# Performance work log

Hardware: AMD Instinct MI355X
Metric: run time of the kernel (lower is better)

The kernel has to match this reference:

```python
import jax, jax.numpy as jnp
import numpy as np

B, T, I, H, C = 8192, 28, 28, 128, 10


def setup_inputs() -> dict:
    key = jax.random.key(0)
    ks = jax.random.split(key, 7)
    s_ih = 1.0 / np.sqrt(H)
    return {
        "x": jax.random.normal(ks[0], (B, T, I), dtype=jnp.float32),
        "W_ih": jax.random.normal(ks[1], (4 * H, I), dtype=jnp.float32) * s_ih,
        "W_hh": jax.random.normal(ks[2], (4 * H, H), dtype=jnp.float32) * s_ih,
        "b_ih": jax.random.normal(ks[3], (4 * H,), dtype=jnp.float32) * s_ih,
        "b_hh": jax.random.normal(ks[4], (4 * H,), dtype=jnp.float32) * s_ih,
        "W_fc": jax.random.normal(ks[5], (C, H), dtype=jnp.float32) * s_ih,
        "b_fc": jnp.zeros((C,), dtype=jnp.float32),
    }


def reference(x, W_ih, W_hh, b_ih, b_hh, W_fc, b_fc):
    # x: [B, T, I]. PyTorch LSTM gate order: i, f, g, o.
    b = b_ih + b_hh  # [4H]
    # Precompute input projections for all timesteps: [T, B, 4H]
    x_proj = jnp.einsum("bti,gi->tbg", x, W_ih) + b
    h0 = jnp.zeros((x.shape[0], H), dtype=x.dtype)
    c0 = jnp.zeros_like(h0)

    def step(carry, xp_t):
        h, c = carry
        gates = xp_t + h @ W_hh.T  # [B, 4H]
        i_g, f_g, g_g, o_g = jnp.split(gates, 4, axis=-1)
        i_g = jax.nn.sigmoid(i_g)
        f_g = jax.nn.sigmoid(f_g)
        g_g = jnp.tanh(g_g)
        o_g = jax.nn.sigmoid(o_g)
        c = f_g * c + i_g * g_g
        h = o_g * jnp.tanh(c)
        return (h, c), None

    (h_last, _), _ = jax.lax.scan(step, (h0, c0), x_proj)
    # outputs[:, -1, :] == final hidden state; fc + relu
    return jax.nn.relu(h_last @ W_fc.T + b_fc)
```

## Files before the change

kernel.cpp:

```cpp
#include <hip/hip_runtime.h>
#include <math.h>

typedef __attribute__((ext_vector_type(8))) _Float16 half8;
typedef __attribute__((ext_vector_type(4))) _Float16 half4;
typedef __attribute__((ext_vector_type(4))) float    f32x4;
typedef __attribute__((ext_vector_type(2))) float    f32x2;

#define TSTEPS 28
#define IDIM   28
#define HDIM   128
#define NKC    5
#define TILE_B 32
#define CDIM   10

#if __has_builtin(__builtin_amdgcn_exp2f)
#define EXP2F(x) __builtin_amdgcn_exp2f(x)
#else
#define EXP2F(x) exp2f(x)
#endif
#if __has_builtin(__builtin_amdgcn_rcpf)
#define RCPF(x) __builtin_amdgcn_rcpf(x)
#else
#define RCPF(x) (1.0f / (x))
#endif

#define NLOG2E (-1.44269504f)
#define P2LOG2E (2.88539008f)

__global__ __launch_bounds__(256) void pack_w(const float* __restrict__ Wih,
                                              const float* __restrict__ Whh,
                                              const float* __restrict__ bih,
                                              const float* __restrict__ bhh,
                                              _Float16* __restrict__ P) {
    int e = blockIdx.x * 256 + threadIdx.x;
    if (e >= NKC * 4 * 8 * 64 * 8) return;
    int j  = e & 7;
    int ln = (e >> 3) & 63;
    int w  = (e >> 9) & 7;
    int t  = (e >> 12) & 3;
    int kc = e >> 14;
    int k  = kc * 32 + ((ln >> 4) << 3) + j;
    int u  = w * 16 + (ln & 15);
    int g  = t * HDIM + u;
    float v = 0.f;
    if (k < HDIM)                   v = Whh[g * HDIM + k];
    else if (k < HDIM + IDIM)       v = Wih[g * IDIM + (k - HDIM)];
    else if (k == HDIM + IDIM)      v = bih[g] + bhh[g];
    float sc = (t == 2) ? P2LOG2E : NLOG2E;
    P[e] = (_Float16)(v * sc);
}

__global__ __launch_bounds__(512, 2) void lstm_kernel(
    const float* __restrict__ x,
    const _Float16* __restrict__ P,
    const float* __restrict__ Wfc,
    const float* __restrict__ b_fc,
    float* __restrict__ out)
{
    __shared__ __align__(16) _Float16 frag[2][NKC][64][8];
    __shared__ __align__(16) float hplain[TILE_B][HDIM + 4];

    const int tid = threadIdx.x;
    const int l   = tid & 63;
    const int w   = tid >> 6;
    const int b0  = blockIdx.x * TILE_B;

    half8 breg[4][4];
    half8 breg4[4];
    {
        const half8* Pp = (const half8*)P;
        #pragma unroll
        for (int kc = 0; kc < 4; ++kc)
            #pragma unroll
            for (int t4 = 0; t4 < 4; ++t4)
                breg[t4][kc] = Pp[((kc * 4 + t4) * 8 + w) * 64 + l];
        #pragma unroll
        for (int t4 = 0; t4 < 4; ++t4)
            breg4[t4] = Pp[((4 * 4 + t4) * 8 + w) * 64 + l];
    }

    {
        float4 z = {0.f, 0.f, 0.f, 0.f};
        if (tid < 256) {
            ((float4*)frag)[tid] = z;
            ((float4*)frag)[320 + tid] = z;
        }
    }
    if (tid < 32) {
        int g = tid >> 4, i = tid & 15;
        half4 onev = {(_Float16)1.f, (_Float16)0.f, (_Float16)0.f, (_Float16)0.f};
        *(half4*)&frag[g][4][48 + i][4] = onev;
    }

    const bool xact = (l < 14);
    const int xid   = w * 14 + l;
    const int xrow  = xid / 7, xg = xid % 7;
    const int xslot = xrow + 16 * (xg >> 1);
    const int xoff  = (xg & 1) * 4;
    const float4* xsA = (const float4*)(x + (size_t)(b0 + xrow) * (TSTEPS * IDIM));
    const float4* xsB = (const float4*)(x + (size_t)(b0 + 16 + xrow) * (TSTEPS * IDIM));
    float4 xh;
    if (xact) {
        float4 xa0 = xsA[xg];
        float4 xb0 = xsB[xg];
        half4 ha = {(_Float16)xa0.x, (_Float16)xa0.y, (_Float16)xa0.z, (_Float16)xa0.w};
        half4 hb = {(_Float16)xb0.x, (_Float16)xb0.y, (_Float16)xb0.z, (_Float16)xb0.w};
        *(half4*)&frag[0][4][xslot][xoff] = ha;
        *(half4*)&frag[1][4][xslot][xoff] = hb;
        xh = xsA[7 + xg];
    }

    f32x2 cA01 = {0.f, 0.f}, cA23 = {0.f, 0.f};
    f32x2 cB01 = {0.f, 0.f}, cB23 = {0.f, 0.f};
    const int u    = w * 16 + (l & 15);
    const int kc_h = w >> 1;
    const int quad = (2 * w + ((l >> 3) & 1)) & 3;
    const int jh   = l & 7;
    const int mb   = (l >> 4) << 2;

    f32x4 acc_A[4], acc_B[4];

    auto activation = [&](f32x4 (&g4)[4], f32x2 &c01, f32x2 &c23,
                          _Float16 (*fragA)[64][8], bool lastT, int rowbase) {
        float hv[4];
        #pragma unroll
        for (int rp = 0; rp < 2; ++rp) {
            const int r0 = rp * 2, r1 = r0 + 1;
            f32x2 Ei = {EXP2F(g4[0][r0]), EXP2F(g4[0][r1])};
            f32x2 Ef = {EXP2F(g4[1][r0]), EXP2F(g4[1][r1])};
            f32x2 Eg = {EXP2F(g4[2][r0]), EXP2F(g4[2][r1])};
            f32x2 Eo = {EXP2F(g4[3][r0]), EXP2F(g4[3][r1])};
            f32x2 one = {1.f, 1.f};
            f32x2 Di = Ei + one, Df = Ef + one, Dg = Eg + one, Do = Eo + one;
            f32x2 Pif = Di * Df, Pgo = Dg * Do;
            f32x2 Rif = {RCPF(Pif.x), RCPF(Pif.y)};
            f32x2 Rgo = {RCPF(Pgo.x), RCPF(Pgo.y)};
            f32x2 is = Rif * Df, fs = Rif * Di;
            f32x2 gt = one - 2.f * (Rgo * Do);
            f32x2 os = Rgo * Dg;
            f32x2 cstp = rp ? c23 : c01;
            f32x2 c = fs * cstp + is * gt;
            if (rp) c23 = c; else c01 = c;
            f32x2 Etc = {EXP2F(c.x * P2LOG2E), EXP2F(c.y * P2LOG2E)};
            f32x2 Dtc = Etc + one;
            f32x2 Rtc = {RCPF(Dtc.x), RCPF(Dtc.y)};
            f32x2 tc = one - 2.f * Rtc;
            f32x2 h2 = os * tc;
            hv[r0] = h2.x; hv[r1] = h2.y;
        }
        #pragma unroll
        for (int r = 0; r < 4; ++r) {
            fragA[kc_h][mb + r + 16 * quad][jh] = (_Float16)hv[r];
            if (lastT) hplain[rowbase + mb + r][u] = hv[r];
        }
    };

    auto run_phase = [&](f32x4 (&accM)[4], _Float16 (*fragM)[64][8],
                         f32x4 (&accA)[4], _Float16 (*fragA)[64][8],
                         f32x2 &c01, f32x2 &c23, int rowbase,
                         bool doAct, bool doKc4, bool lastT) {
        half8 a[4];
        #pragma unroll
        for (int kc = 0; kc < 4; ++kc)
            a[kc] = *(const half8*)&fragM[kc][l][0];
        half8 a4;
        if (doKc4) a4 = *(const half8*)&fragA[4][l][0];
        #pragma unroll
        for (int t4 = 0; t4 < 4; ++t4)
            #pragma unroll
            for (int kc = 0; kc < 4; ++kc)
                accM[t4] = __builtin_amdgcn_mfma_f32_16x16x32_f16(a[kc], breg[t4][kc], accM[t4], 0, 0, 0);
        if (doAct) activation(accA, c01, c23, fragA, lastT, rowbase);
        if (doKc4) {
            #pragma unroll
            for (int t4 = 0; t4 < 4; ++t4) { f32x4 z = {0.f, 0.f, 0.f, 0.f}; accA[t4] = z; }
            #pragma unroll
            for (int t4 = 0; t4 < 4; ++t4)
                accA[t4] = __builtin_amdgcn_mfma_f32_16x16x32_f16(a4, breg4[t4], accA[t4], 0, 0, 0);
        }
    };

    __syncthreads();

    {
        half8 aA4 = *(const half8*)&frag[0][4][l][0];
        #pragma unroll
        for (int t4 = 0; t4 < 4; ++t4) { f32x4 z = {0.f, 0.f, 0.f, 0.f}; acc_A[t4] = z; }
        #pragma unroll
        for (int t4 = 0; t4 < 4; ++t4)
            acc_A[t4] = __builtin_amdgcn_mfma_f32_16x16x32_f16(aA4, breg4[t4], acc_A[t4], 0, 0, 0);
    }
    __syncthreads();

    for (int t = 0; t < TSTEPS; ++t) {
        const bool more = (t + 1 < TSTEPS);

        if (xact && more) {
            half4 hc = {(_Float16)xh.x, (_Float16)xh.y, (_Float16)xh.z, (_Float16)xh.w};
            *(half4*)&frag[0][4][xslot][xoff] = hc;
        }
        run_phase(acc_A, frag[0], acc_B, frag[1], cB01, cB23, 16,
                  t > 0, true, false);
        if (xact && more) xh = xsB[(t + 1) * 7 + xg];
        __syncthreads();

        if (xact && more) {
            half4 hc = {(_Float16)xh.x, (_Float16)xh.y, (_Float16)xh.z, (_Float16)xh.w};
            *(half4*)&frag[1][4][xslot][xoff] = hc;
        }
        run_phase(acc_B, frag[1], acc_A, frag[0], cA01, cA23, 0,
                  true, more, !more);
        if (xact && t + 2 < TSTEPS) xh = xsA[(t + 2) * 7 + xg];
        __syncthreads();
    }

    activation(acc_B, cB01, cB23, frag[1], true, 16);
    __syncthreads();

    if (tid < TILE_B * CDIM) {
        int row = tid / CDIM, c = tid % CDIM;
        const float4* hv4 = (const float4*)&hplain[row][0];
        const float4* wf  = (const float4*)(Wfc + c * HDIM);
        float s = b_fc[c];
        #pragma unroll
        for (int q = 0; q < 32; ++q) {
            float4 a4 = hv4[q], b4 = wf[q];
            s += a4.x * b4.x + a4.y * b4.y + a4.z * b4.z + a4.w * b4.w;
        }
        out[(size_t)(b0 + row) * CDIM + c] = fmaxf(s, 0.f);
    }
}

extern "C" void kernel_launch(void* const* d_in, const int* in_sizes, int n_in,
                              void* d_out, int out_size, void* d_ws, size_t ws_size,
                              hipStream_t stream) {
    const float* x   = (const float*)d_in[0];
    const float* Wih = (const float*)d_in[1];
    const float* Whh = (const float*)d_in[2];
    const float* bih = (const float*)d_in[3];
    const float* bhh = (const float*)d_in[4];
    const float* Wfc = (const float*)d_in[5];
    const float* bfc = (const float*)d_in[6];
    float* out = (float*)d_out;
    _Float16* P = (_Float16*)d_ws;

    hipLaunchKernelGGL(pack_w, dim3(320), dim3(256), 0, stream, Wih, Whh, bih, bhh, P);
    hipLaunchKernelGGL(lstm_kernel, dim3(8192 / TILE_B), dim3(512), 0, stream,
                       x, P, Wfc, bfc, out);
}
```

Before: 130.2 us.

## Interleave gate MFMAs with activation math and peel first/last LSTM phases

Restructures the ping-pong LSTM step so the other tile's activation work is split into row-pair chunks placed between the per-gate MFMA chains. Sched_group_barrier hints enforce an MFMA/VALU/DS interleave. The first and last phases are peeled out of the loop, so the steady-state body has no conditional flags. This aims to hide transcendental and VALU latency under matrix-core work, at the cost of more code and fragile compiler scheduling hints that could raise register pressure.

```diff
diff --git a/kernel.cpp b/kernel.cpp
--- a/kernel.cpp
+++ b/kernel.cpp
@@ -23,9 +23,29 @@
 #else
 #define RCPF(x) (1.0f / (x))
 #endif
+#if __has_builtin(__builtin_amdgcn_sched_group_barrier)
+#define SGB(m,n) __builtin_amdgcn_sched_group_barrier((m),(n),0)
+#else
+#define SGB(m,n)
+#endif
 
 #define NLOG2E (-1.44269504f)
 #define P2LOG2E (2.88539008f)
+
+#define MFMA16(a,b,c) __builtin_amdgcn_mfma_f32_16x16x32_f16((a),(b),(c),0,0,0)
+
+#define SGB_PIPE_FULL() do {            \
+    SGB(0x100, 5);                      \
+    SGB(0x400, 8); SGB(0x002, 12);      \
+    SGB(0x008, 4);                      \
+    SGB(0x400, 8); SGB(0x002, 12);      \
+    SGB(0x008, 4);                      \
+    SGB(0x400, 8); SGB(0x002, 12);      \
+    SGB(0x008, 4);                      \
+    SGB(0x400, 8); SGB(0x002, 12);      \
+    SGB(0x008, 4);                      \
+    SGB(0x008, 4);                      \
+} while (0)
 
 __global__ __launch_bounds__(256) void pack_w(const float* __restrict__ Wih,
                                               const float* __restrict__ Whh,
@@ -119,102 +139,157 @@
     const int mb   = (l >> 4) << 2;
 
     f32x4 acc_A[4], acc_B[4];
-
-    auto activation = [&](f32x4 (&g4)[4], f32x2 &c01, f32x2 &c23,
-                          _Float16 (*fragA)[64][8], bool lastT, int rowbase) {
+    const f32x4 zc = {0.f, 0.f, 0.f, 0.f};
+
+    auto act_rp = [&](f32x4 (&g4)[4], f32x2 &cst, int rp, float* hv) {
+        const int r0 = rp * 2, r1 = r0 + 1;
+        f32x2 Ei = {EXP2F(g4[0][r0]), EXP2F(g4[0][r1])};
+        f32x2 Ef = {EXP2F(g4[1][r0]), EXP2F(g4[1][r1])};
+        f32x2 Eg = {EXP2F(g4[2][r0]), EXP2F(g4[2][r1])};
+        f32x2 Eo = {EXP2F(g4[3][r0]), EXP2F(g4[3][r1])};
+        f32x2 one = {1.f, 1.f};
+        f32x2 Di = Ei + one, Df = Ef + one, Dg = Eg + one, Do = Eo + one;
+        f32x2 Pif = Di * Df, Pgo = Dg * Do;
+        f32x2 Rif = {RCPF(Pif.x), RCPF(Pif.y)};
+        f32x2 Rgo = {RCPF(Pgo.x), RCPF(Pgo.y)};
+        f32x2 is = Rif * Df, fs = Rif * Di;
+        f32x2 gt = one - 2.f * (Rgo * Do);
+        f32x2 os = Rgo * Dg;
+        f32x2 c = fs * cst + is * gt;
+        cst = c;
+        f32x2 Etc = {EXP2F(c.x * P2LOG2E), EXP2F(c.y * P2LOG2E)};
+        f32x2 Dtc = Etc + one;
+        f32x2 Rtc = {RCPF(Dtc.x), RCPF(Dtc.y)};
+        f32x2 tc = one - 2.f * Rtc;
+        f32x2 h2 = os * tc;
+        hv[r0] = h2.x; hv[r1] = h2.y;
+    };
+
+    auto phase_full = [&](f32x4 (&accM)[4], _Float16 (*fragM)[64][8],
+                          f32x4 (&accA)[4], _Float16 (*fragA)[64][8],
+                          f32x2 &c01, f32x2 &c23) {
+        half8 a0 = *(const half8*)&fragM[0][l][0];
+        half8 a1 = *(const half8*)&fragM[1][l][0];
+        half8 a2 = *(const half8*)&fragM[2][l][0];
+        half8 a3 = *(const half8*)&fragM[3][l][0];
+        half8 a4 = *(const half8*)&fragA[4][l][0];
         float hv[4];
-        #pragma unroll
-        for (int rp = 0; rp < 2; ++rp) {
-            const int r0 = rp * 2, r1 = r0 + 1;
-            f32x2 Ei = {EXP2F(g4[0][r0]), EXP2F(g4[0][r1])};
-            f32x2 Ef = {EXP2F(g4[1][r0]), EXP2F(g4[1][r1])};
-            f32x2 Eg = {EXP2F(g4[2][r0]), EXP2F(g4[2][r1])};
-            f32x2 Eo = {EXP2F(g4[3][r0]), EXP2F(g4[3][r1])};
-            f32x2 one = {1.f, 1.f};
-            f32x2 Di = Ei + one, Df = Ef + one, Dg = Eg + one, Do = Eo + one;
-            f32x2 Pif = Di * Df, Pgo = Dg * Do;
-            f32x2 Rif = {RCPF(Pif.x), RCPF(Pif.y)};
-            f32x2 Rgo = {RCPF(Pgo.x), RCPF(Pgo.y)};
-            f32x2 is = Rif * Df, fs = Rif * Di;
-            f32x2 gt = one - 2.f * (Rgo * Do);
-            f32x2 os = Rgo * Dg;
-            f32x2 cstp = rp ? c23 : c01;
-            f32x2 c = fs * cstp + is * gt;
-            if (rp) c23 = c; else c01 = c;
-            f32x2 Etc = {EXP2F(c.x * P2LOG2E), EXP2F(c.y * P2LOG2E)};
-            f32x2 Dtc = Etc + one;
-            f32x2 Rtc = {RCPF(Dtc.x), RCPF(Dtc.y)};
-            f32x2 tc = one - 2.f * Rtc;
-            f32x2 h2 = os * tc;
-            hv[r0] = h2.x; hv[r1] = h2.y;
-        }
-        #pragma unroll
-        for (int r = 0; r < 4; ++r) {
+        accM[0] = MFMA16(a0, breg[0][0], accM[0]);
+        accM[0] = MFMA16(a1, breg[0][1], accM[0]);
+        accM[0] = MFMA16(a2, breg[0][2], accM[0]);
+        accM[0] = MFMA16(a3, breg[0][3], accM[0]);
+        act_rp(accA, c01, 0, hv);
+        accM[1] = MFMA16(a0, breg[1][0], accM[1]);
+        accM[1] = MFMA16(a1, breg[1][1], accM[1]);
+        accM[1] = MFMA16(a2, breg[1][2], accM[1]);
+        accM[1] = MFMA16(a3, breg[1][3], accM[1]);
+        act_rp(accA, c23, 1, hv);
+        accM[2] = MFMA16(a0, breg[2][0], accM[2]);
+        accM[2] = MFMA16(a1, breg[2][1], accM[2]);
+        accM[2] = MFMA16(a2, breg[2][2], accM[2]);
+        accM[2] = MFMA16(a3, breg[2][3], accM[2]);
+        #pragma unroll
+        for (int r = 0; r < 4; ++r)
             fragA[kc_h][mb + r + 16 * quad][jh] = (_Float16)hv[r];
-            if (lastT) hplain[rowbase + mb + r][u] = hv[r];
-        }
+        accM[3] = MFMA16(a0, breg[3][0], accM[3]);
+        accM[3] = MFMA16(a1, breg[3][1], accM[3]);
+        accM[3] = MFMA16(a2, breg[3][2], accM[3]);
+        accM[3] = MFMA16(a3, breg[3][3], accM[3]);
+        #pragma unroll
+        for (int t4 = 0; t4 < 4; ++t4)
+            accA[t4] = MFMA16(a4, breg4[t4], zc);
+        SGB_PIPE_FULL();
     };
 
-    auto run_phase = [&](f32x4 (&accM)[4], _Float16 (*fragM)[64][8],
-                         f32x4 (&accA)[4], _Float16 (*fragA)[64][8],
-                         f32x2 &c01, f32x2 &c23, int rowbase,
-                         bool doAct, bool doKc4, bool lastT) {
-        half8 a[4];
-        #pragma unroll
-        for (int kc = 0; kc < 4; ++kc)
-            a[kc] = *(const half8*)&fragM[kc][l][0];
-        half8 a4;
-        if (doKc4) a4 = *(const half8*)&fragA[4][l][0];
+    __syncthreads();
+
+    {
+        half8 aA4 = *(const half8*)&frag[0][4][l][0];
         #pragma unroll
         for (int t4 = 0; t4 < 4; ++t4)
-            #pragma unroll
-            for (int kc = 0; kc < 4; ++kc)
-                accM[t4] = __builtin_amdgcn_mfma_f32_16x16x32_f16(a[kc], breg[t4][kc], accM[t4], 0, 0, 0);
-        if (doAct) activation(accA, c01, c23, fragA, lastT, rowbase);
-        if (doKc4) {
-            #pragma unroll
-            for (int t4 = 0; t4 < 4; ++t4) { f32x4 z = {0.f, 0.f, 0.f, 0.f}; accA[t4] = z; }
-            #pragma unroll
-            for (int t4 = 0; t4 < 4; ++t4)
-                accA[t4] = __builtin_amdgcn_mfma_f32_16x16x32_f16(a4, breg4[t4], accA[t4], 0, 0, 0);
-        }
-    };
-
+            acc_A[t4] = MFMA16(aA4, breg4[t4], zc);
+    }
     __syncthreads();
 
-    {
-        half8 aA4 = *(const half8*)&frag[0][4][l][0];
-        #pragma unroll
-        for (int t4 = 0; t4 < 4; ++t4) { f32x4 z = {0.f, 0.f, 0.f, 0.f}; acc_A[t4] = z; }
+    if (xact) {
+        half4 hc = {(_Float16)xh.x, (_Float16)xh.y, (_Float16)xh.z, (_Float16)xh.w};
+        *(half4*)&frag[0][4][xslot][xoff] = hc;
+    }
+    {
+        half8 a0 = *(const half8*)&frag[0][0][l][0];
+        half8 a1 = *(const half8*)&frag[0][1][l][0];
+        half8 a2 = *(const half8*)&frag[0][2][l][0];
+        half8 a3 = *(const half8*)&frag[0][3][l][0];
+        half8 a4 = *(const half8*)&frag[1][4][l][0];
+        #pragma unroll
+        for (int t4 = 0; t4 < 4; ++t4) {
+            acc_A[t4] = MFMA16(a0, breg[t4][0], acc_A[t4]);
+            acc_A[t4] = MFMA16(a1, breg[t4][1], acc_A[t4]);
+            acc_A[t4] = MFMA16(a2, breg[t4][2], acc_A[t4]);
+            acc_A[t4] = MFMA16(a3, breg[t4][3], acc_A[t4]);
+        }
         #pragma unroll
         for (int t4 = 0; t4 < 4; ++t4)
-            acc_A[t4] = __builtin_amdgcn_mfma_f32_16x16x32_f16(aA4, breg4[t4], acc_A[t4], 0, 0, 0);
-    }
+            acc_B[t4] = MFMA16(a4, breg4[t4], zc);
+    }
+    if (xact) xh = xsB[7 + xg];
     __syncthreads();
 
-    for (int t = 0; t < TSTEPS; ++t) {
-        const bool more = (t + 1 < TSTEPS);
-
-        if (xact && more) {
+    for (int t = 0; t < TSTEPS - 1; ++t) {
+        if (xact) {
+            half4 hc = {(_Float16)xh.x, (_Float16)xh.y, (_Float16)xh.z, (_Float16)xh.w};
+            *(half4*)&frag[1][4][xslot][xoff] = hc;
+        }
+        phase_full(acc_B, frag[1], acc_A, frag[0], cA01, cA23);
+        if (xact && t + 2 < TSTEPS) xh = xsA[(t + 2) * 7 + xg];
+        __syncthreads();
+
+        if (xact && t + 2 < TSTEPS) {
             half4 hc = {(_Float16)xh.x, (_Float16)xh.y, (_Float16)xh.z, (_Float16)xh.w};
             *(half4*)&frag[0][4][xslot][xoff] = hc;
         }
-        run_phase(acc_A, frag[0], acc_B, frag[1], cB01, cB23, 16,
-                  t > 0, true, false);
-        if (xact && more) xh = xsB[(t + 1) * 7 + xg];
+        phase_full(acc_A, frag[0], acc_B, frag[1], cB01, cB23);
+        if (xact && t + 2 < TSTEPS) xh = xsB[(t + 2) * 7 + xg];
         __syncthreads();
-
-        if (xact && more) {
-            half4 hc = {(_Float16)xh.x, (_Float16)xh.y, (_Float16)xh.z, (_Float16)xh.w};
-            *(half4*)&frag[1][4][xslot][xoff] = hc;
-        }
-        run_phase(acc_B, frag[1], acc_A, frag[0], cA01, cA23, 0,
-                  true, more, !more);
-        if (xact && t + 2 < TSTEPS) xh = xsA[(t + 2) * 7 + xg];
-        __syncthreads();
-    }
-
-    activation(acc_B, cB01, cB23, frag[1], true, 16);
+    }
+
+    {
+        half8 a0 = *(const half8*)&frag[1][0][l][0];
+        half8 a1 = *(const half8*)&frag[1][1][l][0];
+        half8 a2 = *(const half8*)&frag[1][2][l][0];
+        half8 a3 = *(const half8*)&frag[1][3][l][0];
+        float hv[4];
+        acc_B[0] = MFMA16(a0, breg[0][0], acc_B[0]);
+        acc_B[0] = MFMA16(a1, breg[0][1], acc_B[0]);
+        acc_B[0] = MFMA16(a2, breg[0][2], acc_B[0]);
+        acc_B[0] = MFMA16(a3, breg[0][3], acc_B[0]);
+        act_rp(acc_A, cA01, 0, hv);
+        acc_B[1] = MFMA16(a0, breg[1][0], acc_B[1]);
+        acc_B[1] = MFMA16(a1, breg[1][1], acc_B[1]);
+        acc_B[1] = MFMA16(a2, breg[1][2], acc_B[1]);
+        acc_B[1] = MFMA16(a3, breg[1][3], acc_B[1]);
+        act_rp(acc_A, cA23, 1, hv);
+        acc_B[2] = MFMA16(a0, breg[2][0], acc_B[2]);
+        acc_B[2] = MFMA16(a1, breg[2][1], acc_B[2]);
+        acc_B[2] = MFMA16(a2, breg[2][2], acc_B[2]);
+        acc_B[2] = MFMA16(a3, breg[2][3], acc_B[2]);
+        #pragma unroll
+        for (int r = 0; r < 4; ++r)
+            hplain[mb + r][u] = hv[r];
+        acc_B[3] = MFMA16(a0, breg[3][0], acc_B[3]);
+        acc_B[3] = MFMA16(a1, breg[3][1], acc_B[3]);
+        acc_B[3] = MFMA16(a2, breg[3][2], acc_B[3]);
+        acc_B[3] = MFMA16(a3, breg[3][3], acc_B[3]);
+    }
+
+    {
+        float hv[4];
+        act_rp(acc_B, cB01, 0, hv);
+        act_rp(acc_B, cB23, 1, hv);
+        #pragma unroll
+        for (int r = 0; r < 4; ++r)
+            hplain[16 + mb + r][u] = hv[r];
+    }
     __syncthreads();
 
     if (tid < TILE_B * CDIM) {
```

Measured after the change: 128.9 us. About the same (-1.0%).
